# Kernel tuning notes

Measured on AMD Instinct MI355X. Metric: run time of the kernel, lower is better.

Reference implementation:

```python
import jax, jax.numpy as jnp
import numpy as np

N_NODES = 50000
N_EDGES = 800000
NEG_SLOPE = 0.2


def _gat_layer(x, src, dst, W, a_src, a_dst, bias, heads, out_ch):
    """PyG-style GATConv with self-loops already appended to src/dst."""
    N = x.shape[0]
    h = (x @ W.T).reshape(N, heads, out_ch)            # [N,H,C]
    alpha_src = jnp.einsum('nhc,hc->nh', h, a_src)      # [N,H]
    alpha_dst = jnp.einsum('nhc,hc->nh', h, a_dst)      # [N,H]
    e = jax.nn.leaky_relu(alpha_src[src] + alpha_dst[dst], NEG_SLOPE)  # [E,H]
    # segment softmax over incoming edges of each destination node
    m = jax.ops.segment_max(e, dst, num_segments=N)     # [N,H]
    ex = jnp.exp(e - m[dst])
    denom = jax.ops.segment_sum(ex, dst, num_segments=N)  # [N,H] (>0: self-loops)
    alpha = ex / (denom[dst] + 1e-16)                    # [E,H]
    out = jax.ops.segment_sum(h[src] * alpha[:, :, None], dst, num_segments=N)  # [N,H,C]
    return out.reshape(N, heads * out_ch) + bias


def _with_self_loops(edge_index, n):
    loop = jnp.arange(n, dtype=edge_index.dtype)
    src = jnp.concatenate([edge_index[0], loop])
    dst = jnp.concatenate([edge_index[1], loop])
    return src, dst


def setup_inputs() -> dict:
    key = jax.random.key(0)
    ks = jax.random.split(key, 12)
    s = lambda fan: 1.0 / np.sqrt(fan)
    return {
        'x': jax.random.normal(ks[0], (N_NODES, 16), jnp.float32),
        'edge_index': jax.random.randint(ks[1], (2, N_EDGES), 0, N_NODES, jnp.int64),
        'W1': jax.random.normal(ks[2], (256, 16), jnp.float32) * s(16),
        'att_src1': jax.random.normal(ks[3], (4, 64), jnp.float32) * s(64),
        'att_dst1': jax.random.normal(ks[4], (4, 64), jnp.float32) * s(64),
        'b1': jnp.zeros((256,), jnp.float32),
        'W2': jax.random.normal(ks[5], (64, 256), jnp.float32) * s(256),
        'att_src2': jax.random.normal(ks[6], (1, 64), jnp.float32) * s(64),
        'att_dst2': jax.random.normal(ks[7], (1, 64), jnp.float32) * s(64),
        'b2': jnp.zeros((64,), jnp.float32),
        'fc_w': jax.random.normal(ks[8], (1, 64), jnp.float32) * s(64),
        'fc_b': jnp.zeros((1,), jnp.float32),
    }


def reference(x, edge_index, W1, att_src1, att_dst1, b1,
              W2, att_src2, att_dst2, b2, fc_w, fc_b):
    src, dst = _with_self_loops(edge_index, x.shape[0])
    h = jax.nn.elu(_gat_layer(x, src, dst, W1, att_src1, att_dst1, b1, heads=4, out_ch=64))
    h = jax.nn.elu(_gat_layer(h, src, dst, W2, att_src2, att_dst2, b2, heads=1, out_ch=64))
    return h @ fc_w.T + fc_b
```

## Files before the change

kernel.cpp:

```cpp
#include <hip/hip_runtime.h>
#include <hip/hip_bf16.h>
#include <stdint.h>

#define N_NODES 50000
#define N_EDGES 800000
#define MAXDEG  96
#define NSLICE  6250
#define NSB     196

#define OFF_X    0
#define OFF_W1   800000
#define OFF_AS1  804096
#define OFF_AD1  804352
#define OFF_B1   804608
#define OFF_W2   804864
#define OFF_AS2  821248
#define OFF_AD2  821312
#define OFF_B2   821376
#define OFF_FCW  821440
#define OFF_FCB  821504
#define N_CANON  821505
#define N_W2B    16384
#define N_W1B    16384
#define N_CONV   (N_CANON + N_W2B + N_W1B + N_NODES)

#define TSTRIDE 264

typedef __hip_bfloat16 bf16;
typedef __attribute__((ext_vector_type(8))) short short8;
typedef __attribute__((ext_vector_type(4))) float f32x4;

__device__ __forceinline__ float b2f(bf16 v){ return (float)v; }
__device__ __forceinline__ int clampi(int v, int lo, int hi){ return v < lo ? lo : (v > hi ? hi : v); }
__device__ __forceinline__ float clampf(float v){ return fminf(fmaxf(v, -40.f), 40.f); }
__device__ __forceinline__ uint16_t f2bfbits(float f){
  union { float f; uint32_t u; } c; c.f = f;
  uint32_t r = c.u + 0x7fff + ((c.u >> 16) & 1);
  return (uint16_t)(r >> 16);
}
__device__ __forceinline__ float bitsf(uint32_t u){
  union { uint32_t u; float f; } c; c.u = u; return c.f;
}
__device__ __forceinline__ uint32_t fbits(float f){
  union { float f; uint32_t u; } c; c.f = f; return c.u;
}

__device__ __forceinline__ int load_src(const int* ei, int i, int f){
  return f ? ei[2*(size_t)i] : ei[i];
}
__device__ __forceinline__ int load_dst(const int* ei, int i, int f){
  return f ? ei[2*((size_t)N_EDGES + i)] : ei[N_EDGES + i];
}

__global__ void k_detect(const int* __restrict__ ei, const uint16_t* __restrict__ xu,
                         int* __restrict__ flag){
  const int l = threadIdx.x;
  int or_odd = ei[2*l + 1] | ei[2*(400000 + l) + 1];
  int hits = 0;
  for(int k = 0; k < 64; k++){
    int e = (xu[l*64 + k] >> 7) & 0xFF;
    hits += (e >= 200);
  }
  #pragma unroll
  for(int off=32; off; off>>=1){
    or_odd |= __shfl_xor(or_odd, off, 64);
    hits   += __shfl_xor(hits,   off, 64);
  }
  if(l == 0){
    flag[0] = (or_odd == 0) ? 1 : 0;
    flag[1] = (hits > 16) ? 1 : 0;
  }
}

__global__ void k_convert(const void* x, const void* W1, const void* as1w, const void* ad1w,
                          const void* b1, const void* W2, const void* as2w, const void* ad2w,
                          const void* b2, const void* fcw, const void* fcb,
                          float* __restrict__ canon, uint16_t* __restrict__ W2b,
                          uint16_t* __restrict__ W1b, int* __restrict__ cnt,
                          int* __restrict__ csr_pad, const int* __restrict__ flag){
  int i = blockIdx.x*256 + threadIdx.x;
  int fp32 = flag[1];
  if(i >= N_CANON + N_W2B + N_W1B){
    int j = i - (N_CANON + N_W2B + N_W1B);
    if(j < N_NODES){ cnt[j] = 1; csr_pad[(size_t)j*MAXDEG] = j; }
    return;
  }
  if(i >= N_CANON + N_W2B){
    int j2 = i - (N_CANON + N_W2B);
    int j = j2 >> 6, kk = j2 & 63;
    uint16_t v = 0;
    if((kk >> 4) == (j >> 6)){
      int e = j*16 + (kk & 15);
      v = fp32 ? f2bfbits(((const float*)W1)[e]) : ((const uint16_t*)W1)[e];
    }
    W1b[j2] = v;
    return;
  }
  if(i >= N_CANON){
    int j = i - N_CANON;
    W2b[j] = fp32 ? f2bfbits(((const float*)W2)[j]) : ((const uint16_t*)W2)[j];
    return;
  }
  const void* src; int off;
  if     (i < OFF_W1 ){ src = x;    off = i; }
  else if(i < OFF_AS1){ src = W1;   off = i - OFF_W1; }
  else if(i < OFF_AD1){ src = as1w; off = i - OFF_AS1; }
  else if(i < OFF_B1 ){ src = ad1w; off = i - OFF_AD1; }
  else if(i < OFF_W2 ){ src = b1;   off = i - OFF_B1; }
  else if(i < OFF_AS2){ src = W2;   off = i - OFF_W2; }
  else if(i < OFF_AD2){ src = as2w; off = i - OFF_AS2; }
  else if(i < OFF_B2 ){ src = ad2w; off = i - OFF_AD2; }
  else if(i < OFF_FCW){ src = b2;   off = i - OFF_B2; }
  else if(i < OFF_FCB){ src = fcw;  off = i - OFF_FCW; }
  else               { src = fcb;  off = 0; }
  float v = fp32 ? ((const float*)src)[off] : b2f(((const bf16*)src)[off]);
  canon[i] = v;
}


__global__ __launch_bounds__(256) void k_prepscat(const float* __restrict__ canon,
                        uint32_t* __restrict__ pack, float* __restrict__ dpack,
                        const int* __restrict__ ei, int* __restrict__ cnt,
                        int* __restrict__ csr_pad, const int* __restrict__ flag){
  const int tid = threadIdx.x;
  if(blockIdx.x >= 196){
    const int bid = blockIdx.x - 196;
    const int grp = bid & 7, sb = bid >> 3;
    const int f = flag[0];
    const int lo = grp*NSLICE, hi = lo + NSLICE;
    const int base = sb*4096;
    #pragma unroll 4
    for(int j = 0; j < 16; j++){
      int i = base + j*256 + tid;
      if(i >= N_EDGES) break;
      int d = clampi(load_dst(ei, i, f), 0, N_NODES-1);
      if(d >= lo && d < hi){
        int s = clampi(load_src(ei, i, f), 0, N_NODES-1);
        int pos = atomicAdd(&cnt[d], 1);
        pos = clampi(pos, 0, MAXDEG-1);
        csr_pad[(size_t)d*MAXDEG + pos] = s;
      }
    }
    return;
  }
  __shared__ float ps[64], pd[64];
  if(tid < 128){
    int e = tid & 63;
    int h = e >> 4, k = e & 15;
    const float* av = canon + (tid < 64 ? OFF_AS1 : OFF_AD1) + h*64;
    const float* Wp = canon + OFF_W1 + (h*64)*16 + k;
    float acc = 0.f;
    #pragma unroll 8
    for(int c = 0; c < 64; c++) acc += av[c] * Wp[c*16];
    (tid < 64 ? ps : pd)[e] = acc;
  }
  __syncthreads();
  int n = blockIdx.x*256 + tid;
  if(n >= N_NODES) return;
  float xr[16];
  const float4* xp = (const float4*)(canon + OFF_X + n*16);
  #pragma unroll
  for(int t=0;t<4;t++){ float4 v = xp[t]; xr[4*t]=v.x; xr[4*t+1]=v.y; xr[4*t+2]=v.z; xr[4*t+3]=v.w; }
  uint32_t w[16];
  #pragma unroll
  for(int t=0;t<8;t++)
    w[t] = (uint32_t)f2bfbits(xr[2*t]) | ((uint32_t)f2bfbits(xr[2*t+1]) << 16);
  float qs[8];
  #pragma unroll
  for(int h=0;h<4;h++){
    float a=0.f, b=0.f;
    #pragma unroll
    for(int k=0;k<16;k++){ a += ps[h*16+k]*xr[k]; b += pd[h*16+k]*xr[k]; }
    a = clampf(a); b = clampf(b);
    w[8+2*h]  = fbits(__expf(a));
    w[9+2*h]  = fbits(__expf(0.2f*a));
    qs[2*h]   = __expf(b);
    qs[2*h+1] = __expf(0.2f*b);
  }
  uint4* dst = (uint4*)(pack + (size_t)n*16);
  dst[0] = make_uint4(w[0],w[1],w[2],w[3]);
  dst[1] = make_uint4(w[4],w[5],w[6],w[7]);
  dst[2] = make_uint4(w[8],w[9],w[10],w[11]);
  dst[3] = make_uint4(w[12],w[13],w[14],w[15]);
  float4* dd = (float4*)(dpack + (size_t)n*8);
  dd[0] = make_float4(qs[0],qs[1],qs[2],qs[3]);
  dd[1] = make_float4(qs[4],qs[5],qs[6],qs[7]);
}


struct Acc { float y0,y1,y2,y3,d0,d1,d2,d3; };

__device__ __forceinline__ void batch8(const int* __restrict__ csr, int i0, const char* pk,
                                       float2 qq, int g, int k, int h3, int base, Acc& a){
  int iA = csr[i0 + g], iB = csr[i0 + 4 + g];
  const char* rA = pk + (size_t)iA*64;
  const char* rB = pk + (size_t)iB*64;
  float xvA = bitsf((uint32_t)(*(const uint16_t*)(rA + k*2)) << 16);
  float2 ppA = *(const float2*)(rA + 32 + h3*8);
  float xvB = bitsf((uint32_t)(*(const uint16_t*)(rB + k*2)) << 16);
  float2 ppB = *(const float2*)(rB + 32 + h3*8);
  float wA = fmaxf(ppA.x*qq.x, ppA.y*qq.y);
  float wB = fmaxf(ppB.x*qq.x, ppB.y*qq.y);
  float a0 = __shfl(wA, base|0, 64), a1 = __shfl(wA, base|1, 64);
  float a2 = __shfl(wA, base|2, 64), a3 = __shfl(wA, base|3, 64);
  float b0 = __shfl(wB, base|0, 64), b1 = __shfl(wB, base|1, 64);
  float b2 = __shfl(wB, base|2, 64), b3 = __shfl(wB, base|3, 64);
  a.y0 += a0*xvA + b0*xvB; a.d0 += a0 + b0;
  a.y1 += a1*xvA + b1*xvB; a.d1 += a1 + b1;
  a.y2 += a2*xvA + b2*xvB; a.d2 += a2 + b2;
  a.y3 += a3*xvA + b3*xvB; a.d3 += a3 + b3;
}

__device__ __forceinline__ void tail8(const int* __restrict__ csr, int i0, int end, const char* pk,
                                      float2 qq, int g, int k, int h3, int base, Acc& a){
  int iiA = i0 + g, iiB = i0 + 4 + g;
  bool vA = iiA < end, vB = iiB < end;
  int iA = csr[vA ? iiA : end-1];
  int iB = csr[vB ? iiB : end-1];
  const char* rA = pk + (size_t)iA*64;
  const char* rB = pk + (size_t)iB*64;
  float xvA = bitsf((uint32_t)(*(const uint16_t*)(rA + k*2)) << 16);
  float2 ppA = *(const float2*)(rA + 32 + h3*8);
  float xvB = bitsf((uint32_t)(*(const uint16_t*)(rB + k*2)) << 16);
  float2 ppB = *(const float2*)(rB + 32 + h3*8);
  float wA = vA ? fmaxf(ppA.x*qq.x, ppA.y*qq.y) : 0.f;
  float wB = vB ? fmaxf(ppB.x*qq.x, ppB.y*qq.y) : 0.f;
  float a0 = __shfl(wA, base|0, 64), a1 = __shfl(wA, base|1, 64);
  float a2 = __shfl(wA, base|2, 64), a3 = __shfl(wA, base|3, 64);
  float b0 = __shfl(wB, base|0, 64), b1 = __shfl(wB, base|1, 64);
  float b2 = __shfl(wB, base|2, 64), b3 = __shfl(wB, base|3, 64);
  a.y0 += a0*xvA + b0*xvB; a.d0 += a0 + b0;
  a.y1 += a1*xvA + b1*xvB; a.d1 += a1 + b1;
  a.y2 += a2*xvA + b2*xvB; a.d2 += a2 + b2;
  a.y3 += a3*xvA + b3*xvB; a.d3 += a3 + b3;
}

__device__ __forceinline__ void store_y(Acc& a, int n, int g, int k, uint16_t* __restrict__ yb){
  a.y0 += __shfl_xor(a.y0,16,64); a.y0 += __shfl_xor(a.y0,32,64);
  a.y1 += __shfl_xor(a.y1,16,64); a.y1 += __shfl_xor(a.y1,32,64);
  a.y2 += __shfl_xor(a.y2,16,64); a.y2 += __shfl_xor(a.y2,32,64);
  a.y3 += __shfl_xor(a.y3,16,64); a.y3 += __shfl_xor(a.y3,32,64);
  a.d0 += __shfl_xor(a.d0,16,64); a.d0 += __shfl_xor(a.d0,32,64);
  a.d1 += __shfl_xor(a.d1,16,64); a.d1 += __shfl_xor(a.d1,32,64);
  a.d2 += __shfl_xor(a.d2,16,64); a.d2 += __shfl_xor(a.d2,32,64);
  a.d3 += __shfl_xor(a.d3,16,64); a.d3 += __shfl_xor(a.d3,32,64);
  float yH = (g==0) ? a.y0 : (g==1) ? a.y1 : (g==2) ? a.y2 : a.y3;
  float dH = (g==0) ? a.d0 : (g==1) ? a.d1 : (g==2) ? a.d2 : a.d3;
  yb[(size_t)n*64 + g*16 + k] = f2bfbits(yH / (dH + 1e-16f));
}

__global__ __launch_bounds__(256) void k_aggy(const int* __restrict__ cnt, const int* __restrict__ csr_pad,
                       const uint32_t* __restrict__ pack, const float* __restrict__ dpack,
                       uint16_t* __restrict__ yb){
  const int wv = threadIdx.x >> 6, lane = threadIdx.x & 63;
  const int g = lane >> 4, k = lane & 15, h3 = k & 3;
  const int base = lane & 48;
  const char* pk = (const char*)pack;

  for(int np = blockIdx.x*4 + wv; np < N_NODES/2; np += gridDim.x*4){
    const int nA = np*2, nB = np*2 + 1;
    const int begA = nA*MAXDEG, endA = begA + cnt[nA];
    const int begB = nB*MAXDEG, endB = begB + cnt[nB];
    const float2 qqA = *(const float2*)(dpack + (size_t)nA*8 + h3*2);
    const float2 qqB = *(const float2*)(dpack + (size_t)nB*8 + h3*2);
    Acc aA = {0,0,0,0,0,0,0,0}, aB = {0,0,0,0,0,0,0,0};
    int iA = begA, iB = begB;
    while(iA + 8 <= endA && iB + 8 <= endB){
      batch8(csr_pad, iA, pk, qqA, g, k, h3, base, aA);
      batch8(csr_pad, iB, pk, qqB, g, k, h3, base, aB);
      iA += 8; iB += 8;
    }
    while(iA + 8 <= endA){ batch8(csr_pad, iA, pk, qqA, g, k, h3, base, aA); iA += 8; }
    while(iB + 8 <= endB){ batch8(csr_pad, iB, pk, qqB, g, k, h3, base, aB); iB += 8; }
    if(iA < endA) tail8(csr_pad, iA, endA, pk, qqA, g, k, h3, base, aA);
    if(iB < endB) tail8(csr_pad, iB, endB, pk, qqB, g, k, h3, base, aB);
    store_y(aA, nA, g, k, yb);
    store_y(aB, nB, g, k, yb);
  }
}


__global__ __launch_bounds__(64, 4) void k_mlp(const uint16_t* __restrict__ yb,
                        const uint16_t* __restrict__ W1b, const uint16_t* __restrict__ W2b,
                        const float* __restrict__ canon,
                        bf16* __restrict__ h2, float2* __restrict__ pq2, float2* __restrict__ dq2){
  __shared__ uint16_t tl[16*TSTRIDE];
  const int lane = threadIdx.x & 63;
  const int quad = lane >> 4, c = lane & 15;
  const int n0 = blockIdx.x * 16;

  float b1v[16];
  #pragma unroll
  for(int cb=0; cb<16; cb++) b1v[cb] = canon[OFF_B1 + cb*16 + c];
  float asj[4], adj[4];
  #pragma unroll
  for(int cb=0; cb<4; cb++){
    asj[cb] = canon[OFF_AS2 + cb*16 + c];
    adj[cb] = canon[OFF_AD2 + cb*16 + c];
  }

  short8 af0 = *(const short8*)(yb + (size_t)(n0 + c)*64 + quad*8);
  short8 af1 = *(const short8*)(yb + (size_t)(n0 + c)*64 + 32 + quad*8);
  #pragma unroll
  for(int cb=0; cb<16; cb++){
    short8 wf = *(const short8*)(W1b + (cb*16 + c)*64 + (cb>>3)*32 + quad*8);
    f32x4 acc = (f32x4){0.f,0.f,0.f,0.f};
    acc = __builtin_amdgcn_mfma_f32_16x16x32_bf16((cb>>3) ? af1 : af0, wf, acc, 0,0,0);
    #pragma unroll
    for(int r=0; r<4; r++){
      float o = acc[r] + b1v[cb];
      o = (o > 0.f) ? o : (__expf(o) - 1.f);
      tl[(quad*4 + r)*TSTRIDE + cb*16 + c] = f2bfbits(o);
    }
  }
  f32x4 acc2[4];
  #pragma unroll
  for(int cb=0; cb<4; cb++) acc2[cb] = (f32x4){0.f,0.f,0.f,0.f};
  #pragma unroll
  for(int ks=0; ks<8; ks++){
    short8 af = *(const short8*)(tl + c*TSTRIDE + ks*32 + quad*8);
    #pragma unroll
    for(int cb=0; cb<4; cb++){
      short8 bfrag = *(const short8*)(W2b + (cb*16 + c)*256 + ks*32 + quad*8);
      acc2[cb] = __builtin_amdgcn_mfma_f32_16x16x32_bf16(af, bfrag, acc2[cb], 0,0,0);
    }
  }
  float vs[4] = {0.f,0.f,0.f,0.f}, vd[4] = {0.f,0.f,0.f,0.f};
  #pragma unroll
  for(int cb=0; cb<4; cb++)
    #pragma unroll
    for(int r=0; r<4; r++){
      float v = acc2[cb][r];
      h2[(size_t)(n0 + quad*4 + r)*64 + cb*16 + c] = __float2bfloat16(v);
      vs[r] += v * asj[cb];
      vd[r] += v * adj[cb];
    }
  #pragma unroll
  for(int r=0; r<4; r++){
    #pragma unroll
    for(int off=1; off<16; off<<=1){
      vs[r] += __shfl_xor(vs[r], off, 64);
      vd[r] += __shfl_xor(vd[r], off, 64);
    }
  }
  if(c == 0){
    #pragma unroll
    for(int r=0; r<4; r++){
      float s = clampf(vs[r]), d = clampf(vd[r]);
      pq2[n0 + quad*4 + r] = make_float2(__expf(s), __expf(0.2f*s));
      dq2[n0 + quad*4 + r] = make_float2(__expf(d), __expf(0.2f*d));
    }
  }
}


__global__ __launch_bounds__(256) void k_agg2(const int* __restrict__ cnt, const int* __restrict__ csr_pad,
                       const bf16* __restrict__ h2, const float2* __restrict__ pq2,
                       const float2* __restrict__ dq2, const float* __restrict__ canon,
                       void* __restrict__ outv, const int* __restrict__ flag){
  const int wv = threadIdx.x >> 6, lane = threadIdx.x & 63;
  const int g = lane >> 4, k = lane & 15;
  const char* h2b = (const char*)h2;
  float4 b2v = ((const float4*)(canon + OFF_B2))[k];
  float4 fcv = ((const float4*)(canon + OFF_FCW))[k];
  const float fcb0 = canon[OFF_FCB];
  const int ofp32 = flag[1];
  for(int n = blockIdx.x*4 + wv; n < N_NODES; n += gridDim.x*4){
    const int beg = n*MAXDEG, end = beg + cnt[n];
    const float2 qn = dq2[n];
    float a0=0.f,a1=0.f,a2=0.f,a3=0.f, den=0.f;
    int i0 = beg;
    const int nfull = (end - beg) >> 3;
    if(nfull > 0){
      int iA = csr_pad[i0 + g], iB = csr_pad[i0 + 4 + g];
      for(int b = 1; b < nfull; b++){
        int nA = csr_pad[i0 + 8 + g], nB = csr_pad[i0 + 12 + g];
        uint2 hA = *(const uint2*)(h2b + (size_t)iA*128 + k*8);
        float2 pA = pq2[iA];
        uint2 hB = *(const uint2*)(h2b + (size_t)iB*128 + k*8);
        float2 pB = pq2[iB];
        float wA = fmaxf(pA.x*qn.x, pA.y*qn.y);
        float wB = fmaxf(pB.x*qn.x, pB.y*qn.y);
        den += wA + wB;
        a0 += wA*bitsf(hA.x << 16) + wB*bitsf(hB.x << 16);
        a1 += wA*bitsf(hA.x & 0xffff0000u) + wB*bitsf(hB.x & 0xffff0000u);
        a2 += wA*bitsf(hA.y << 16) + wB*bitsf(hB.y << 16);
        a3 += wA*bitsf(hA.y & 0xffff0000u) + wB*bitsf(hB.y & 0xffff0000u);
        iA = nA; iB = nB;
        i0 += 8;
      }
      {
        uint2 hA = *(const uint2*)(h2b + (size_t)iA*128 + k*8);
        float2 pA = pq2[iA];
        uint2 hB = *(const uint2*)(h2b + (size_t)iB*128 + k*8);
        float2 pB = pq2[iB];
        float wA = fmaxf(pA.x*qn.x, pA.y*qn.y);
        float wB = fmaxf(pB.x*qn.x, pB.y*qn.y);
        den += wA + wB;
        a0 += wA*bitsf(hA.x << 16) + wB*bitsf(hB.x << 16);
        a1 += wA*bitsf(hA.x & 0xffff0000u) + wB*bitsf(hB.x & 0xffff0000u);
        a2 += wA*bitsf(hA.y << 16) + wB*bitsf(hB.y << 16);
        a3 += wA*bitsf(hA.y & 0xffff0000u) + wB*bitsf(hB.y & 0xffff0000u);
        i0 += 8;
      }
    }
    if(i0 < end){
      int iiA = i0 + g, iiB = i0 + 4 + g;
      bool vA = iiA < end, vB = iiB < end;
      int iA = csr_pad[vA ? iiA : end-1];
      int iB = csr_pad[vB ? iiB : end-1];
      uint2 hA = *(const uint2*)(h2b + (size_t)iA*128 + k*8);
      float2 pA = pq2[iA];
      uint2 hB = *(const uint2*)(h2b + (size_t)iB*128 + k*8);
      float2 pB = pq2[iB];
      float wA = vA ? fmaxf(pA.x*qn.x, pA.y*qn.y) : 0.f;
      float wB = vB ? fmaxf(pB.x*qn.x, pB.y*qn.y) : 0.f;
      den += wA + wB;
      a0 += wA*bitsf(hA.x << 16) + wB*bitsf(hB.x << 16);
      a1 += wA*bitsf(hA.x & 0xffff0000u) + wB*bitsf(hB.x & 0xffff0000u);
      a2 += wA*bitsf(hA.y << 16) + wB*bitsf(hB.y << 16);
      a3 += wA*bitsf(hA.y & 0xffff0000u) + wB*bitsf(hB.y & 0xffff0000u);
    }
    a0 += __shfl_xor(a0,16,64); a0 += __shfl_xor(a0,32,64);
    a1 += __shfl_xor(a1,16,64); a1 += __shfl_xor(a1,32,64);
    a2 += __shfl_xor(a2,16,64); a2 += __shfl_xor(a2,32,64);
    a3 += __shfl_xor(a3,16,64); a3 += __shfl_xor(a3,32,64);
    den += __shfl_xor(den,16,64); den += __shfl_xor(den,32,64);
    float inv = 1.f/(den + 1e-16f);
    float o0 = a0*inv + b2v.x, o1 = a1*inv + b2v.y;
    float o2 = a2*inv + b2v.z, o3 = a3*inv + b2v.w;
    o0 = (o0>0.f)?o0:expm1f(o0); o1 = (o1>0.f)?o1:expm1f(o1);
    o2 = (o2>0.f)?o2:expm1f(o2); o3 = (o3>0.f)?o3:expm1f(o3);
    float v = o0*fcv.x + o1*fcv.y + o2*fcv.z + o3*fcv.w;
    v += __shfl_xor(v,1,64); v += __shfl_xor(v,2,64);
    v += __shfl_xor(v,4,64); v += __shfl_xor(v,8,64);
    if(lane == 0){
      float r = v + fcb0;
      if(ofp32) ((float*)outv)[n] = r;
      else      ((bf16*)outv)[n] = __float2bfloat16(r);
    }
  }
}


extern "C" void kernel_launch(void* const* d_in, const int* in_sizes, int n_in,
                              void* d_out, int out_size, void* d_ws, size_t ws_size,
                              hipStream_t stream){
  (void)in_sizes; (void)n_in; (void)out_size;
  const int* ei = (const int*)d_in[1];

  char* w = (char*)d_ws;
  auto carve = [&](size_t bytes)->char*{ char* p = w; w += (bytes + 255) & ~(size_t)255; return p; };
  int*      cnt     = (int*)     carve((size_t)N_NODES*4);
  int*      flag    = (int*)     carve(256);
  int*      csr_pad = (int*)     carve((size_t)N_NODES*MAXDEG*4);
  float*    canon   = (float*)   carve((size_t)N_CANON*4);
  uint16_t* W2b     = (uint16_t*)carve((size_t)N_W2B*2);
  uint16_t* W1b     = (uint16_t*)carve((size_t)N_W1B*2);
  uint32_t* pack    = (uint32_t*)carve((size_t)N_NODES*64);
  float*    dpack   = (float*)   carve((size_t)N_NODES*32);
  uint16_t* yb      = (uint16_t*)carve((size_t)N_NODES*64*2);
  float2*   pq2     = (float2*)  carve((size_t)N_NODES*8);
  float2*   dq2     = (float2*)  carve((size_t)N_NODES*8);
  bf16*     h2      = (bf16*)    carve((size_t)N_NODES*64*2);
  size_t required = (size_t)(w - (char*)d_ws);
  if(ws_size < required) return;

  hipLaunchKernelGGL(k_detect,   dim3(1), dim3(64), 0, stream, ei, (const uint16_t*)d_in[0], flag);
  hipLaunchKernelGGL(k_convert,  dim3((N_CONV+255)/256), dim3(256), 0, stream,
                     d_in[0], d_in[2], d_in[3], d_in[4], d_in[5], d_in[6], d_in[7], d_in[8],
                     d_in[9], d_in[10], d_in[11], canon, W2b, W1b, cnt, csr_pad, flag);
  hipLaunchKernelGGL(k_prepscat, dim3(196 + 8*NSB), dim3(256), 0, stream,
                     canon, pack, dpack, ei, cnt, csr_pad, flag);
  hipLaunchKernelGGL(k_aggy,     dim3(2048), dim3(256), 0, stream, cnt, csr_pad, pack, dpack, yb);
  hipLaunchKernelGGL(k_mlp,      dim3(N_NODES/16), dim3(64), 0, stream, yb, W1b, W2b, canon, h2, pq2, dq2);
  hipLaunchKernelGGL(k_agg2,     dim3(2048), dim3(256), 0, stream, cnt, csr_pad, h2, pq2, dq2, canon, d_out, flag);
}
```

Measured before the change: 201.8 us.

## Fuse layer-1 aggregation with MLP into one persistent kernel via LDS

Merges the layer-1 neighbor aggregation kernel and the dense MLP kernel into one persistent kernel. Each block aggregates 16 nodes into shared memory and then runs both bf16 MFMA GEMMs from LDS, with W1/W2 fragments held in registers for the block's lifetime. This removes the global yb round trip, one kernel launch and the repeated per-block weight loads. In exchange it adds block-wide barriers between the irregular gather phase and the MFMA phase, so load imbalance across the 16 nodes stalls the whole block, and the grid shrinks to 1024 blocks.

```diff
diff --git a/kernel.cpp b/kernel.cpp
--- a/kernel.cpp
+++ b/kernel.cpp
@@ -25,6 +25,7 @@
 #define N_CONV   (N_CANON + N_W2B + N_W1B + N_NODES)
 
 #define TSTRIDE 264
+#define YSTRIDE 72
 
 typedef __hip_bfloat16 bf16;
 typedef __attribute__((ext_vector_type(8))) short short8;
@@ -235,7 +236,8 @@
   a.y3 += a3*xvA + b3*xvB; a.d3 += a3 + b3;
 }
 
-__device__ __forceinline__ void store_y(Acc& a, int n, int g, int k, uint16_t* __restrict__ yb){
+__device__ __forceinline__ void store_y_lds(Acc& a, int nl, int g, int k,
+                                            uint16_t* __restrict__ ybt){
   a.y0 += __shfl_xor(a.y0,16,64); a.y0 += __shfl_xor(a.y0,32,64);
   a.y1 += __shfl_xor(a.y1,16,64); a.y1 += __shfl_xor(a.y1,32,64);
   a.y2 += __shfl_xor(a.y2,16,64); a.y2 += __shfl_xor(a.y2,32,64);
@@ -246,109 +248,111 @@
   a.d3 += __shfl_xor(a.d3,16,64); a.d3 += __shfl_xor(a.d3,32,64);
   float yH = (g==0) ? a.y0 : (g==1) ? a.y1 : (g==2) ? a.y2 : a.y3;
   float dH = (g==0) ? a.d0 : (g==1) ? a.d1 : (g==2) ? a.d2 : a.d3;
-  yb[(size_t)n*64 + g*16 + k] = f2bfbits(yH / (dH + 1e-16f));
-}
-
-__global__ __launch_bounds__(256) void k_aggy(const int* __restrict__ cnt, const int* __restrict__ csr_pad,
-                       const uint32_t* __restrict__ pack, const float* __restrict__ dpack,
-                       uint16_t* __restrict__ yb){
-  const int wv = threadIdx.x >> 6, lane = threadIdx.x & 63;
-  const int g = lane >> 4, k = lane & 15, h3 = k & 3;
-  const int base = lane & 48;
+  ybt[nl*YSTRIDE + g*16 + k] = f2bfbits(yH / (dH + 1e-16f));
+}
+
+
+__global__ __launch_bounds__(256) void k_aggmlp(
+    const int* __restrict__ cnt, const int* __restrict__ csr_pad,
+    const uint32_t* __restrict__ pack, const float* __restrict__ dpack,
+    const uint16_t* __restrict__ W1b, const uint16_t* __restrict__ W2b,
+    const float* __restrict__ canon,
+    bf16* __restrict__ h2, float2* __restrict__ pq2, float2* __restrict__ dq2){
+  __shared__ uint16_t ybt[16*YSTRIDE];
+  __shared__ uint16_t tile[16*TSTRIDE];
+  __shared__ float vsred[4][16], vdred[4][16];
+  const int tid = threadIdx.x, w = tid >> 6, lane = tid & 63;
+  const int g = lane >> 4, k = lane & 15, h3 = k & 3, base = lane & 48;
+  const int quad = g, c = k;
+  const int hf = w >> 1;
   const char* pk = (const char*)pack;
 
-  for(int np = blockIdx.x*4 + wv; np < N_NODES/2; np += gridDim.x*4){
-    const int nA = np*2, nB = np*2 + 1;
-    const int begA = nA*MAXDEG, endA = begA + cnt[nA];
-    const int begB = nB*MAXDEG, endB = begB + cnt[nB];
-    const float2 qqA = *(const float2*)(dpack + (size_t)nA*8 + h3*2);
-    const float2 qqB = *(const float2*)(dpack + (size_t)nB*8 + h3*2);
-    Acc aA = {0,0,0,0,0,0,0,0}, aB = {0,0,0,0,0,0,0,0};
-    int iA = begA, iB = begB;
-    while(iA + 8 <= endA && iB + 8 <= endB){
-      batch8(csr_pad, iA, pk, qqA, g, k, h3, base, aA);
-      batch8(csr_pad, iB, pk, qqB, g, k, h3, base, aB);
-      iA += 8; iB += 8;
-    }
-    while(iA + 8 <= endA){ batch8(csr_pad, iA, pk, qqA, g, k, h3, base, aA); iA += 8; }
-    while(iB + 8 <= endB){ batch8(csr_pad, iB, pk, qqB, g, k, h3, base, aB); iB += 8; }
-    if(iA < endA) tail8(csr_pad, iA, endA, pk, qqA, g, k, h3, base, aA);
-    if(iB < endB) tail8(csr_pad, iB, endB, pk, qqB, g, k, h3, base, aB);
-    store_y(aA, nA, g, k, yb);
-    store_y(aB, nB, g, k, yb);
-  }
-}
-
-
-__global__ __launch_bounds__(64, 4) void k_mlp(const uint16_t* __restrict__ yb,
-                        const uint16_t* __restrict__ W1b, const uint16_t* __restrict__ W2b,
-                        const float* __restrict__ canon,
-                        bf16* __restrict__ h2, float2* __restrict__ pq2, float2* __restrict__ dq2){
-  __shared__ uint16_t tl[16*TSTRIDE];
-  const int lane = threadIdx.x & 63;
-  const int quad = lane >> 4, c = lane & 15;
-  const int n0 = blockIdx.x * 16;
-
-  float b1v[16];
-  #pragma unroll
-  for(int cb=0; cb<16; cb++) b1v[cb] = canon[OFF_B1 + cb*16 + c];
-  float asj[4], adj[4];
-  #pragma unroll
-  for(int cb=0; cb<4; cb++){
-    asj[cb] = canon[OFF_AS2 + cb*16 + c];
-    adj[cb] = canon[OFF_AD2 + cb*16 + c];
-  }
-
-  short8 af0 = *(const short8*)(yb + (size_t)(n0 + c)*64 + quad*8);
-  short8 af1 = *(const short8*)(yb + (size_t)(n0 + c)*64 + 32 + quad*8);
-  #pragma unroll
-  for(int cb=0; cb<16; cb++){
-    short8 wf = *(const short8*)(W1b + (cb*16 + c)*64 + (cb>>3)*32 + quad*8);
-    f32x4 acc = (f32x4){0.f,0.f,0.f,0.f};
-    acc = __builtin_amdgcn_mfma_f32_16x16x32_bf16((cb>>3) ? af1 : af0, wf, acc, 0,0,0);
+  short8 w1f[4]; float b1v[4];
+  #pragma unroll
+  for(int cbl=0; cbl<4; cbl++){
+    int cb = w*4 + cbl;
+    w1f[cbl] = *(const short8*)(W1b + (cb*16 + c)*64 + hf*32 + quad*8);
+    b1v[cbl] = canon[OFF_B1 + cb*16 + c];
+  }
+  short8 w2f[8];
+  #pragma unroll
+  for(int ks=0; ks<8; ks++)
+    w2f[ks] = *(const short8*)(W2b + (w*16 + c)*256 + ks*32 + quad*8);
+  const float asv = canon[OFF_AS2 + w*16 + c];
+  const float adv = canon[OFF_AD2 + w*16 + c];
+
+  for(int t = blockIdx.x; t < N_NODES/16; t += gridDim.x){
+    const int n0 = t*16;
+    #pragma unroll
+    for(int pr=0; pr<2; pr++){
+      const int nA = n0 + w*4 + pr*2, nB = nA + 1;
+      const int begA = nA*MAXDEG, endA = begA + cnt[nA];
+      const int begB = nB*MAXDEG, endB = begB + cnt[nB];
+      const float2 qqA = *(const float2*)(dpack + (size_t)nA*8 + h3*2);
+      const float2 qqB = *(const float2*)(dpack + (size_t)nB*8 + h3*2);
+      Acc aA = {0,0,0,0,0,0,0,0}, aB = {0,0,0,0,0,0,0,0};
+      int iA = begA, iB = begB;
+      while(iA + 8 <= endA && iB + 8 <= endB){
+        batch8(csr_pad, iA, pk, qqA, g, k, h3, base, aA);
+        batch8(csr_pad, iB, pk, qqB, g, k, h3, base, aB);
+        iA += 8; iB += 8;
+      }
+      while(iA + 8 <= endA){ batch8(csr_pad, iA, pk, qqA, g, k, h3, base, aA); iA += 8; }
+      while(iB + 8 <= endB){ batch8(csr_pad, iB, pk, qqB, g, k, h3, base, aB); iB += 8; }
+      if(iA < endA) tail8(csr_pad, iA, endA, pk, qqA, g, k, h3, base, aA);
+      if(iB < endB) tail8(csr_pad, iB, endB, pk, qqB, g, k, h3, base, aB);
+      store_y_lds(aA, w*4 + pr*2,     g, k, ybt);
+      store_y_lds(aB, w*4 + pr*2 + 1, g, k, ybt);
+    }
+    __syncthreads();
+    {
+      short8 af = *(const short8*)(ybt + c*YSTRIDE + hf*32 + quad*8);
+      #pragma unroll
+      for(int cbl=0; cbl<4; cbl++){
+        int cb = w*4 + cbl;
+        f32x4 acc = (f32x4){0.f,0.f,0.f,0.f};
+        acc = __builtin_amdgcn_mfma_f32_16x16x32_bf16(af, w1f[cbl], acc, 0,0,0);
+        #pragma unroll
+        for(int r=0; r<4; r++){
+          float o = acc[r] + b1v[cbl];
+          o = (o > 0.f) ? o : (__expf(o) - 1.f);
+          tile[(quad*4 + r)*TSTRIDE + cb*16 + c] = f2bfbits(o);
+        }
+      }
+    }
+    __syncthreads();
+    f32x4 acc2 = (f32x4){0.f,0.f,0.f,0.f};
+    #pragma unroll
+    for(int ks=0; ks<8; ks++){
+      short8 a2 = *(const short8*)(tile + c*TSTRIDE + ks*32 + quad*8);
+      acc2 = __builtin_amdgcn_mfma_f32_16x16x32_bf16(a2, w2f[ks], acc2, 0,0,0);
+    }
+    float vsp[4], vdp[4];
     #pragma unroll
     for(int r=0; r<4; r++){
-      float o = acc[r] + b1v[cb];
-      o = (o > 0.f) ? o : (__expf(o) - 1.f);
-      tl[(quad*4 + r)*TSTRIDE + cb*16 + c] = f2bfbits(o);
-    }
-  }
-  f32x4 acc2[4];
-  #pragma unroll
-  for(int cb=0; cb<4; cb++) acc2[cb] = (f32x4){0.f,0.f,0.f,0.f};
-  #pragma unroll
-  for(int ks=0; ks<8; ks++){
-    short8 af = *(const short8*)(tl + c*TSTRIDE + ks*32 + quad*8);
-    #pragma unroll
-    for(int cb=0; cb<4; cb++){
-      short8 bfrag = *(const short8*)(W2b + (cb*16 + c)*256 + ks*32 + quad*8);
-      acc2[cb] = __builtin_amdgcn_mfma_f32_16x16x32_bf16(af, bfrag, acc2[cb], 0,0,0);
-    }
-  }
-  float vs[4] = {0.f,0.f,0.f,0.f}, vd[4] = {0.f,0.f,0.f,0.f};
-  #pragma unroll
-  for(int cb=0; cb<4; cb++)
-    #pragma unroll
-    for(int r=0; r<4; r++){
-      float v = acc2[cb][r];
-      h2[(size_t)(n0 + quad*4 + r)*64 + cb*16 + c] = __float2bfloat16(v);
-      vs[r] += v * asj[cb];
-      vd[r] += v * adj[cb];
-    }
-  #pragma unroll
-  for(int r=0; r<4; r++){
-    #pragma unroll
-    for(int off=1; off<16; off<<=1){
-      vs[r] += __shfl_xor(vs[r], off, 64);
-      vd[r] += __shfl_xor(vd[r], off, 64);
-    }
-  }
-  if(c == 0){
-    #pragma unroll
-    for(int r=0; r<4; r++){
-      float s = clampf(vs[r]), d = clampf(vd[r]);
-      pq2[n0 + quad*4 + r] = make_float2(__expf(s), __expf(0.2f*s));
-      dq2[n0 + quad*4 + r] = make_float2(__expf(d), __expf(0.2f*d));
+      float v = acc2[r];
+      h2[(size_t)(n0 + quad*4 + r)*64 + w*16 + c] = __float2bfloat16(v);
+      vsp[r] = v * asv; vdp[r] = v * adv;
+      #pragma unroll
+      for(int off=1; off<16; off<<=1){
+        vsp[r] += __shfl_xor(vsp[r], off, 64);
+        vdp[r] += __shfl_xor(vdp[r], off, 64);
+      }
+    }
+    if(c == 0){
+      #pragma unroll
+      for(int r=0; r<4; r++){
+        vsred[w][quad*4 + r] = vsp[r];
+        vdred[w][quad*4 + r] = vdp[r];
+      }
+    }
+    __syncthreads();
+    if(tid < 16){
+      float s = vsred[0][tid] + vsred[1][tid] + vsred[2][tid] + vsred[3][tid];
+      float d = vdred[0][tid] + vdred[1][tid] + vdred[2][tid] + vdred[3][tid];
+      s = clampf(s); d = clampf(d);
+      pq2[n0 + tid] = make_float2(__expf(s), __expf(0.2f*s));
+      dq2[n0 + tid] = make_float2(__expf(d), __expf(0.2f*d));
     }
   }
 }
@@ -459,7 +463,6 @@
   uint16_t* W1b     = (uint16_t*)carve((size_t)N_W1B*2);
   uint32_t* pack    = (uint32_t*)carve((size_t)N_NODES*64);
   float*    dpack   = (float*)   carve((size_t)N_NODES*32);
-  uint16_t* yb      = (uint16_t*)carve((size_t)N_NODES*64*2);
   float2*   pq2     = (float2*)  carve((size_t)N_NODES*8);
   float2*   dq2     = (float2*)  carve((size_t)N_NODES*8);
   bf16*     h2      = (bf16*)    carve((size_t)N_NODES*64*2);
@@ -472,7 +475,7 @@
                      d_in[9], d_in[10], d_in[11], canon, W2b, W1b, cnt, csr_pad, flag);
   hipLaunchKernelGGL(k_prepscat, dim3(196 + 8*NSB), dim3(256), 0, stream,
                      canon, pack, dpack, ei, cnt, csr_pad, flag);
-  hipLaunchKernelGGL(k_aggy,     dim3(2048), dim3(256), 0, stream, cnt, csr_pad, pack, dpack, yb);
-  hipLaunchKernelGGL(k_mlp,      dim3(N_NODES/16), dim3(64), 0, stream, yb, W1b, W2b, canon, h2, pq2, dq2);
+  hipLaunchKernelGGL(k_aggmlp,   dim3(1024), dim3(256), 0, stream,
+                     cnt, csr_pad, pack, dpack, W1b, W2b, canon, h2, pq2, dq2);
   hipLaunchKernelGGL(k_agg2,     dim3(2048), dim3(256), 0, stream, cnt, csr_pad, h2, pq2, dq2, canon, d_out, flag);
 }
```

After: 215.8 us. 1.07x slower.

## Aggregate one node per wave with prefetched indices and per-lane head weights

Applied to the files above, without the earlier changes.

The aggregation kernel now processes one destination node per wave instead of interleaving two. Each lane computes all four head weights itself from float4 loads of the packed row, which removes the eight cross-lane shuffles per batch. CSR indices for the next batch of eight are loaded before the current batch is accumulated, a software prefetch meant to hide index-load latency. In exchange each lane does redundant weight arithmetic and wider loads, the wave has less independent work in flight, and the degree is now clamped to MAXDEG.

```diff
diff --git a/kernel.cpp b/kernel.cpp
--- a/kernel.cpp
+++ b/kernel.cpp
@@ -188,94 +188,72 @@
 }
 
 
-struct Acc { float y0,y1,y2,y3,d0,d1,d2,d3; };
-
-__device__ __forceinline__ void batch8(const int* __restrict__ csr, int i0, const char* pk,
-                                       float2 qq, int g, int k, int h3, int base, Acc& a){
-  int iA = csr[i0 + g], iB = csr[i0 + 4 + g];
-  const char* rA = pk + (size_t)iA*64;
-  const char* rB = pk + (size_t)iB*64;
-  float xvA = bitsf((uint32_t)(*(const uint16_t*)(rA + k*2)) << 16);
-  float2 ppA = *(const float2*)(rA + 32 + h3*8);
-  float xvB = bitsf((uint32_t)(*(const uint16_t*)(rB + k*2)) << 16);
-  float2 ppB = *(const float2*)(rB + 32 + h3*8);
-  float wA = fmaxf(ppA.x*qq.x, ppA.y*qq.y);
-  float wB = fmaxf(ppB.x*qq.x, ppB.y*qq.y);
-  float a0 = __shfl(wA, base|0, 64), a1 = __shfl(wA, base|1, 64);
-  float a2 = __shfl(wA, base|2, 64), a3 = __shfl(wA, base|3, 64);
-  float b0 = __shfl(wB, base|0, 64), b1 = __shfl(wB, base|1, 64);
-  float b2 = __shfl(wB, base|2, 64), b3 = __shfl(wB, base|3, 64);
-  a.y0 += a0*xvA + b0*xvB; a.d0 += a0 + b0;
-  a.y1 += a1*xvA + b1*xvB; a.d1 += a1 + b1;
-  a.y2 += a2*xvA + b2*xvB; a.d2 += a2 + b2;
-  a.y3 += a3*xvA + b3*xvB; a.d3 += a3 + b3;
-}
-
-__device__ __forceinline__ void tail8(const int* __restrict__ csr, int i0, int end, const char* pk,
-                                      float2 qq, int g, int k, int h3, int base, Acc& a){
-  int iiA = i0 + g, iiB = i0 + 4 + g;
-  bool vA = iiA < end, vB = iiB < end;
-  int iA = csr[vA ? iiA : end-1];
-  int iB = csr[vB ? iiB : end-1];
-  const char* rA = pk + (size_t)iA*64;
-  const char* rB = pk + (size_t)iB*64;
-  float xvA = bitsf((uint32_t)(*(const uint16_t*)(rA + k*2)) << 16);
-  float2 ppA = *(const float2*)(rA + 32 + h3*8);
-  float xvB = bitsf((uint32_t)(*(const uint16_t*)(rB + k*2)) << 16);
-  float2 ppB = *(const float2*)(rB + 32 + h3*8);
-  float wA = vA ? fmaxf(ppA.x*qq.x, ppA.y*qq.y) : 0.f;
-  float wB = vB ? fmaxf(ppB.x*qq.x, ppB.y*qq.y) : 0.f;
-  float a0 = __shfl(wA, base|0, 64), a1 = __shfl(wA, base|1, 64);
-  float a2 = __shfl(wA, base|2, 64), a3 = __shfl(wA, base|3, 64);
-  float b0 = __shfl(wB, base|0, 64), b1 = __shfl(wB, base|1, 64);
-  float b2 = __shfl(wB, base|2, 64), b3 = __shfl(wB, base|3, 64);
-  a.y0 += a0*xvA + b0*xvB; a.d0 += a0 + b0;
-  a.y1 += a1*xvA + b1*xvB; a.d1 += a1 + b1;
-  a.y2 += a2*xvA + b2*xvB; a.d2 += a2 + b2;
-  a.y3 += a3*xvA + b3*xvB; a.d3 += a3 + b3;
-}
-
-__device__ __forceinline__ void store_y(Acc& a, int n, int g, int k, uint16_t* __restrict__ yb){
-  a.y0 += __shfl_xor(a.y0,16,64); a.y0 += __shfl_xor(a.y0,32,64);
-  a.y1 += __shfl_xor(a.y1,16,64); a.y1 += __shfl_xor(a.y1,32,64);
-  a.y2 += __shfl_xor(a.y2,16,64); a.y2 += __shfl_xor(a.y2,32,64);
-  a.y3 += __shfl_xor(a.y3,16,64); a.y3 += __shfl_xor(a.y3,32,64);
-  a.d0 += __shfl_xor(a.d0,16,64); a.d0 += __shfl_xor(a.d0,32,64);
-  a.d1 += __shfl_xor(a.d1,16,64); a.d1 += __shfl_xor(a.d1,32,64);
-  a.d2 += __shfl_xor(a.d2,16,64); a.d2 += __shfl_xor(a.d2,32,64);
-  a.d3 += __shfl_xor(a.d3,16,64); a.d3 += __shfl_xor(a.d3,32,64);
-  float yH = (g==0) ? a.y0 : (g==1) ? a.y1 : (g==2) ? a.y2 : a.y3;
-  float dH = (g==0) ? a.d0 : (g==1) ? a.d1 : (g==2) ? a.d2 : a.d3;
-  yb[(size_t)n*64 + g*16 + k] = f2bfbits(yH / (dH + 1e-16f));
+struct Ay { float y0,y1,y2,y3,d0,d1,d2,d3; };
+
+__device__ __forceinline__ void edge_acc(const char* __restrict__ r, int k,
+                                         float4 qa, float4 qb, bool valid, Ay& a){
+  float xv = bitsf((uint32_t)(*(const uint16_t*)(r + k*2)) << 16);
+  float4 pa = *(const float4*)(r + 32);
+  float4 pb = *(const float4*)(r + 48);
+  float w0 = fmaxf(pa.x*qa.x, pa.y*qa.y);
+  float w1 = fmaxf(pa.z*qa.z, pa.w*qa.w);
+  float w2 = fmaxf(pb.x*qb.x, pb.y*qb.y);
+  float w3 = fmaxf(pb.z*qb.z, pb.w*qb.w);
+  if(!valid){ w0 = 0.f; w1 = 0.f; w2 = 0.f; w3 = 0.f; }
+  a.y0 += w0*xv; a.d0 += w0;
+  a.y1 += w1*xv; a.d1 += w1;
+  a.y2 += w2*xv; a.d2 += w2;
+  a.y3 += w3*xv; a.d3 += w3;
 }
 
 __global__ __launch_bounds__(256) void k_aggy(const int* __restrict__ cnt, const int* __restrict__ csr_pad,
                        const uint32_t* __restrict__ pack, const float* __restrict__ dpack,
                        uint16_t* __restrict__ yb){
   const int wv = threadIdx.x >> 6, lane = threadIdx.x & 63;
-  const int g = lane >> 4, k = lane & 15, h3 = k & 3;
-  const int base = lane & 48;
+  const int g = lane >> 4, k = lane & 15;
   const char* pk = (const char*)pack;
 
-  for(int np = blockIdx.x*4 + wv; np < N_NODES/2; np += gridDim.x*4){
-    const int nA = np*2, nB = np*2 + 1;
-    const int begA = nA*MAXDEG, endA = begA + cnt[nA];
-    const int begB = nB*MAXDEG, endB = begB + cnt[nB];
-    const float2 qqA = *(const float2*)(dpack + (size_t)nA*8 + h3*2);
-    const float2 qqB = *(const float2*)(dpack + (size_t)nB*8 + h3*2);
-    Acc aA = {0,0,0,0,0,0,0,0}, aB = {0,0,0,0,0,0,0,0};
-    int iA = begA, iB = begB;
-    while(iA + 8 <= endA && iB + 8 <= endB){
-      batch8(csr_pad, iA, pk, qqA, g, k, h3, base, aA);
-      batch8(csr_pad, iB, pk, qqB, g, k, h3, base, aB);
-      iA += 8; iB += 8;
-    }
-    while(iA + 8 <= endA){ batch8(csr_pad, iA, pk, qqA, g, k, h3, base, aA); iA += 8; }
-    while(iB + 8 <= endB){ batch8(csr_pad, iB, pk, qqB, g, k, h3, base, aB); iB += 8; }
-    if(iA < endA) tail8(csr_pad, iA, endA, pk, qqA, g, k, h3, base, aA);
-    if(iB < endB) tail8(csr_pad, iB, endB, pk, qqB, g, k, h3, base, aB);
-    store_y(aA, nA, g, k, yb);
-    store_y(aB, nB, g, k, yb);
+  for(int n = blockIdx.x*4 + wv; n < N_NODES; n += gridDim.x*4){
+    const int beg = n*MAXDEG;
+    const int deg = cnt[n];
+    const int end = beg + (deg < MAXDEG ? deg : MAXDEG);
+    const float4 qa = *(const float4*)(dpack + (size_t)n*8);
+    const float4 qb = *(const float4*)(dpack + (size_t)n*8 + 4);
+    Ay a = {0,0,0,0,0,0,0,0};
+    int i0 = beg;
+    const int nfull = (end - beg) >> 3;
+    if(nfull > 0){
+      int iA = csr_pad[i0 + g], iB = csr_pad[i0 + 4 + g];
+      for(int b = 1; b < nfull; b++){
+        int jA = csr_pad[i0 + 8 + g], jB = csr_pad[i0 + 12 + g];
+        edge_acc(pk + (size_t)iA*64, k, qa, qb, true, a);
+        edge_acc(pk + (size_t)iB*64, k, qa, qb, true, a);
+        iA = jA; iB = jB;
+        i0 += 8;
+      }
+      edge_acc(pk + (size_t)iA*64, k, qa, qb, true, a);
+      edge_acc(pk + (size_t)iB*64, k, qa, qb, true, a);
+      i0 += 8;
+    }
+    if(i0 < end){
+      int iiA = i0 + g, iiB = i0 + 4 + g;
+      bool vA = iiA < end, vB = iiB < end;
+      int iA = csr_pad[vA ? iiA : end-1];
+      int iB = csr_pad[vB ? iiB : end-1];
+      edge_acc(pk + (size_t)iA*64, k, qa, qb, vA, a);
+      edge_acc(pk + (size_t)iB*64, k, qa, qb, vB, a);
+    }
+    a.y0 += __shfl_xor(a.y0,16,64); a.y0 += __shfl_xor(a.y0,32,64);
+    a.y1 += __shfl_xor(a.y1,16,64); a.y1 += __shfl_xor(a.y1,32,64);
+    a.y2 += __shfl_xor(a.y2,16,64); a.y2 += __shfl_xor(a.y2,32,64);
+    a.y3 += __shfl_xor(a.y3,16,64); a.y3 += __shfl_xor(a.y3,32,64);
+    a.d0 += __shfl_xor(a.d0,16,64); a.d0 += __shfl_xor(a.d0,32,64);
+    a.d1 += __shfl_xor(a.d1,16,64); a.d1 += __shfl_xor(a.d1,32,64);
+    a.d2 += __shfl_xor(a.d2,16,64); a.d2 += __shfl_xor(a.d2,32,64);
+    a.d3 += __shfl_xor(a.d3,16,64); a.d3 += __shfl_xor(a.d3,32,64);
+    float yH = (g==0) ? a.y0 : (g==1) ? a.y1 : (g==2) ? a.y2 : a.y3;
+    float dH = (g==0) ? a.d0 : (g==1) ? a.d1 : (g==2) ? a.d2 : a.d3;
+    yb[(size_t)n*64 + g*16 + k] = f2bfbits(yH / (dH + 1e-16f));
   }
 }
 
```

New measurement: 200.3 us. About the same (-0.7%).
